# Optimization experiments

Measured on AMD Instinct MI355X. Metric: run time of the kernel, lower is better.

## Reference

```python
import jax, jax.numpy as jnp
import numpy as np


def setup_inputs() -> dict:
    key = jax.random.key(0)
    k1, k2, k3, k4 = jax.random.split(key, 4)
    B, T, E, H = 16, 2048, 1024, 128
    x = jax.random.normal(k1, (B, T, E), dtype=jnp.float32)
    Wk = jax.random.normal(k2, (E, H), dtype=jnp.float32) * (E ** -0.5)
    Wq = jax.random.normal(k3, (E, H), dtype=jnp.float32) * (E ** -0.5)
    Wv = jax.random.normal(k4, (E, H), dtype=jnp.float32) * (E ** -0.5)
    return {"x": x, "Wk": Wk, "Wq": Wq, "Wv": Wv}


def reference(x, Wk, Wq, Wv):
    # x: [B,T,E]; Wk/Wq/Wv: [E,H]
    B, T, E = x.shape
    H = Wk.shape[1]
    k = jnp.einsum('bte,eh->bth', x, Wk)
    q = jnp.einsum('bte,eh->bth', x, Wq)
    v = jnp.einsum('bte,eh->bth', x, Wv)
    # scores [B,T,T]; original masks with -inf THEN scales (equivalent math)
    scores = jnp.einsum('bqh,bkh->bqk', q, k) * (H ** -0.5)
    causal = jnp.tril(jnp.ones((T, T), dtype=bool))
    scores = jnp.where(causal, scores, -jnp.inf)
    weights = jax.nn.softmax(scores, axis=-1)
    # dropout disabled (eval mode reference)
    return jnp.einsum('bqk,bkh->bqh', weights, v)
```

## Files before the change

kernel.cpp:

```cpp
#include <hip/hip_runtime.h>

#define B_ 16
#define T_ 2048
#define E_ 1024
#define H_ 128

typedef short bf16x8 __attribute__((ext_vector_type(8)));
typedef float f32x4 __attribute__((ext_vector_type(4)));
typedef unsigned short u16x4 __attribute__((ext_vector_type(4)));

static __device__ __forceinline__ unsigned short f2bf(float f) {
    unsigned int u = __float_as_uint(f);
    u += 0x7FFFu + ((u >> 16) & 1u);
    return (unsigned short)(u >> 16);
}
static __device__ __forceinline__ unsigned int pk2(unsigned short a, unsigned short b) {
    return (unsigned int)a | ((unsigned int)b << 16);
}
static __device__ __forceinline__ bf16x8 frag(uint4 v) {
    return __builtin_bit_cast(bf16x8, v);
}
static __device__ __forceinline__ void gl16(const unsigned short* g, unsigned short* l) {
    __builtin_amdgcn_global_load_lds(
        (const __attribute__((address_space(1))) void*)g,
        (__attribute__((address_space(3))) void*)l, 16, 0, 0);
}

__global__ __launch_bounds__(256) void cvtw_kernel(
    const float* __restrict__ w0, const float* __restrict__ w1,
    const float* __restrict__ w2, unsigned short* __restrict__ wt)
{
    int g   = blockIdx.x * 256 + threadIdx.x;
    int arr = g >> 14;
    int rem = g & 16383;
    int h   = rem >> 7;
    int e0  = (rem & 127) * 8;
    const float* src = (arr == 0) ? w0 : (arr == 1) ? w1 : w2;
    unsigned short b[8];
#pragma unroll
    for (int i = 0; i < 8; i++) b[i] = f2bf(src[(size_t)(e0 + i) * H_ + h]);
    uint4 o;
    o.x = pk2(b[0], b[1]); o.y = pk2(b[2], b[3]);
    o.z = pk2(b[4], b[5]); o.w = pk2(b[6], b[7]);
    *(uint4*)&wt[(size_t)(arr * 128 + h) * E_ + e0] = o;
}

__global__ __launch_bounds__(512, 2) void proj_kernel(
    const float* __restrict__ x,
    const unsigned short* __restrict__ wt,
    unsigned short* __restrict__ q_ws,
    unsigned short* __restrict__ kp_ws,
    unsigned short* __restrict__ vt_ws)
{
    const int m0 = blockIdx.x * 128;
    __shared__ __align__(16) unsigned short As[2][128 * 32];
    __shared__ __align__(16) unsigned short Bs[2][384 * 32];

    const int tid  = threadIdx.x;
    const int lane = tid & 63;
    const int w    = tid >> 6;
    const int quad = lane >> 4;
    const int lm   = lane & 15;
    const int wr   = (w >> 2) * 64;
    const int wc   = (w & 3) * 96;

    const int srow = tid >> 2;
    const int scol = (tid & 3) * 8;
    const float* gx = x + (size_t)(m0 + srow) * E_ + scol;
    const unsigned short* gw = wt + (size_t)srow * E_ + scol;

    const f32x4 z4 = {0.f, 0.f, 0.f, 0.f};
    f32x4 acc[4][6];
#pragma unroll
    for (int i = 0; i < 4; i++)
#pragma unroll
        for (int j = 0; j < 6; j++) acc[i][j] = z4;

    auto stageB = [&](int kb, int buf) {
        const unsigned short* g = gw + kb * 32;
        unsigned short* l = &Bs[buf][tid * 8];
        gl16(g,                    l);
        gl16(g + (size_t)128 * E_, l + 4096);
        gl16(g + (size_t)256 * E_, l + 8192);
    };
    auto writeA = [&](float4 a0, float4 a1, int buf) {
        uint4 o;
        o.x = pk2(f2bf(a0.x), f2bf(a0.y));
        o.y = pk2(f2bf(a0.z), f2bf(a0.w));
        o.z = pk2(f2bf(a1.x), f2bf(a1.y));
        o.w = pk2(f2bf(a1.z), f2bf(a1.w));
        *(uint4*)&As[buf][srow * 32 + scol] = o;
    };

    float4 a0 = *(const float4*)gx;
    float4 a1 = *(const float4*)(gx + 4);
    stageB(0, 0);
    writeA(a0, a1, 0);
    a0 = *(const float4*)(gx + 32);
    a1 = *(const float4*)(gx + 36);

    for (int kb = 0; kb < 32; kb++) {
        const int cb = kb & 1;
        __syncthreads();

        const int kb2 = (kb + 2 < 32) ? kb + 2 : 31;
        float4 n0 = *(const float4*)(gx + kb2 * 32);
        float4 n1 = *(const float4*)(gx + kb2 * 32 + 4);
        if (kb + 1 < 32) {
            stageB(kb + 1, cb ^ 1);
            writeA(a0, a1, cb ^ 1);
        }

        bf16x8 a[4], b[6];
#pragma unroll
        for (int am = 0; am < 4; am++)
            a[am] = frag(*(const uint4*)&As[cb][(wr + am * 16 + lm) * 32 + quad * 8]);
#pragma unroll
        for (int bn = 0; bn < 6; bn++)
            b[bn] = frag(*(const uint4*)&Bs[cb][(wc + bn * 16 + lm) * 32 + quad * 8]);
#pragma unroll
        for (int am = 0; am < 4; am++)
#pragma unroll
            for (int bn = 0; bn < 6; bn++)
                acc[am][bn] = __builtin_amdgcn_mfma_f32_16x16x32_bf16(
                    a[am], b[bn], acc[am][bn], 0, 0, 0);

        a0 = n0; a1 = n1;
    }

#pragma unroll
    for (int am = 0; am < 4; am++)
#pragma unroll
        for (int bn = 0; bn < 6; bn++) {
            const int gcol  = wc + bn * 16 + lm;
            const int sel   = gcol >> 7;
            const int c     = gcol & 127;
            const int rbase = m0 + wr + am * 16 + quad * 4;
            const int bb    = rbase >> 11;
            const int t     = rbase & 2047;
            if (sel == 0) {
#pragma unroll
                for (int r = 0; r < 4; r++)
                    q_ws[(size_t)(rbase + r) * H_ + c] = f2bf(acc[am][bn][r]);
            } else if (sel == 1) {
#pragma unroll
                for (int r = 0; r < 4; r++) {
                    int tt = t + r;
                    kp_ws[(size_t)(bb * 64 + (tt >> 5)) * 4096 +
                          (c >> 5) * 1024 + (tt & 31) * 32 + (c & 31)] =
                        f2bf(acc[am][bn][r]);
                }
            } else {
                u16x4 pv;
#pragma unroll
                for (int r = 0; r < 4; r++) pv[r] = f2bf(acc[am][bn][r]);
                *(u16x4*)&vt_ws[((size_t)(bb * 64 + (t >> 5)) * 128 + c) * 32 + (t & 31)] = pv;
            }
        }
}

__global__ __launch_bounds__(256, 2) void attn_kernel(
    const unsigned short* __restrict__ q_ws,
    const unsigned short* __restrict__ kp_ws,
    const unsigned short* __restrict__ vt_ws,
    float* __restrict__ out)
{
    __shared__ __align__(16) unsigned short Ks[2][4096];
    __shared__ __align__(16) unsigned short Vs[2][4096];
    __shared__ __align__(16) unsigned short Ps[4][16][40];

    const int bid   = blockIdx.x;
    const int batch = bid & 15;
    const int p     = (bid >> 4) & 15;
    const int tau   = (bid >> 8) ? (31 - p) : p;
    const int nkt   = 2 * tau + 2;

    const int tid  = threadIdx.x;
    const int lane = tid & 63;
    const int ww   = tid >> 6;
    const int quad = lane >> 4;
    const int lm   = lane & 15;
    const float scale = 0.08838834764831845f;

    bf16x8 ones;
#pragma unroll
    for (int i = 0; i < 8; i++) ones[i] = (short)0x3F80;
    const f32x4 z4 = {0.f, 0.f, 0.f, 0.f};

    const size_t bq = (size_t)batch * T_ * H_;
    const int so = ww * 1024 + lane * 8;
    const unsigned short* Kt = kp_ws + (size_t)(batch * 64) * 4096 + so;
    const unsigned short* Vt = vt_ws + (size_t)(batch * 64) * 4096 + so;

    bf16x8 qf[4];
#pragma unroll
    for (int h = 0; h < 4; h++)
        qf[h] = frag(*(const uint4*)(q_ws + bq +
                 (size_t)(tau * 64 + ww * 16 + lm) * H_ + h * 32 + quad * 8));

    f32x4 o[9];
#pragma unroll
    for (int f = 0; f < 9; f++) o[f] = z4;

    gl16(Kt, &Ks[0][ww * 1024]); gl16(Kt + 512, &Ks[0][ww * 1024 + 512]);
    gl16(Vt, &Vs[0][ww * 1024]); gl16(Vt + 512, &Vs[0][ww * 1024 + 512]);

    for (int kt = 0; kt < nkt; kt++) {
        const int cb = kt & 1;
        __syncthreads();

        if (kt + 1 < nkt) {
            const int nb = cb ^ 1;
            const unsigned short* kg = Kt + (size_t)(kt + 1) * 4096;
            const unsigned short* vg = Vt + (size_t)(kt + 1) * 4096;
            gl16(kg, &Ks[nb][ww * 1024]); gl16(kg + 512, &Ks[nb][ww * 1024 + 512]);
            gl16(vg, &Vs[nb][ww * 1024]); gl16(vg + 512, &Vs[nb][ww * 1024 + 512]);
        }

        f32x4 st0 = z4, st1 = z4;
#pragma unroll
        for (int h = 0; h < 4; h++) {
            bf16x8 kf0 = frag(*(const uint4*)&Ks[cb][(h * 32 + lm) * 32 + quad * 8]);
            bf16x8 kf1 = frag(*(const uint4*)&Ks[cb][(h * 32 + 16 + lm) * 32 + quad * 8]);
            st0 = __builtin_amdgcn_mfma_f32_16x16x32_bf16(kf0, qf[h], st0, 0, 0, 0);
            st1 = __builtin_amdgcn_mfma_f32_16x16x32_bf16(kf1, qf[h], st1, 0, 0, 0);
        }

        const int qg = tau * 64 + ww * 16 + lm;
        const int k0 = kt * 32;
        u16x4 pa, pb;
#pragma unroll
        for (int r = 0; r < 4; r++) {
            int kv0 = k0 + quad * 4 + r;
            float e0 = __expf(st0[r] * scale);
            float e1 = __expf(st1[r] * scale);
            pa[r] = (kv0      <= qg) ? f2bf(e0) : (unsigned short)0;
            pb[r] = (kv0 + 16 <= qg) ? f2bf(e1) : (unsigned short)0;
        }
        *(u16x4*)&Ps[ww][lm][quad * 4]      = pa;
        *(u16x4*)&Ps[ww][lm][16 + quad * 4] = pb;
        bf16x8 pf = frag(*(const uint4*)&Ps[ww][lm][quad * 8]);

#pragma unroll
        for (int f = 0; f < 8; f++) {
            bf16x8 vfr = frag(*(const uint4*)&Vs[cb][(f * 16 + lm) * 32 + quad * 8]);
            o[f] = __builtin_amdgcn_mfma_f32_16x16x32_bf16(pf, vfr, o[f], 0, 0, 0);
        }
        o[8] = __builtin_amdgcn_mfma_f32_16x16x32_bf16(pf, ones, o[8], 0, 0, 0);
    }

    float* op = out + bq + (size_t)(tau * 64 + ww * 16) * H_;
#pragma unroll
    for (int r = 0; r < 4; r++) {
        float inv = 1.f / o[8][r];
#pragma unroll
        for (int f = 0; f < 8; f++)
            op[(size_t)(quad * 4 + r) * H_ + f * 16 + lm] = o[f][r] * inv;
    }
}

extern "C" void kernel_launch(void* const* d_in, const int* in_sizes, int n_in,
                              void* d_out, int out_size, void* d_ws, size_t ws_size,
                              hipStream_t stream)
{
    const float* x  = (const float*)d_in[0];
    const float* Wk = (const float*)d_in[1];
    const float* Wq = (const float*)d_in[2];
    const float* Wv = (const float*)d_in[3];
    float* out = (float*)d_out;

    const size_t MH = (size_t)B_ * T_ * H_;
    unsigned short* q_ws  = (unsigned short*)d_ws;
    unsigned short* kp_ws = q_ws + MH;
    unsigned short* vt_ws = kp_ws + MH;
    unsigned short* wt    = vt_ws + MH;

    cvtw_kernel<<<dim3(192), dim3(256), 0, stream>>>(Wq, Wk, Wv, wt);
    proj_kernel<<<dim3(256), dim3(512), 0, stream>>>(x, wt, q_ws, kp_ws, vt_ws);
    attn_kernel<<<dim3(512), dim3(256), 0, stream>>>(q_ws, kp_ws, vt_ws, out);
}
```

Baseline: 281.2 us.

## Shrink projection M-tile, load weight fragments directly from global, add MFMA priority hints

The projection kernel now uses 64-row tiles with 512 blocks. Each wave handles 48 output columns, and weight fragments are read straight from global memory (L2) into registers instead of being staged through shared memory. This removes the large B shared buffer and raises occupancy (launch bounds 4), at the cost of more redundant global weight reads per block and less reuse. The attention kernel also wraps its MFMA sections in s_setprio to favour matrix issue across waves.

```diff
diff --git a/kernel.cpp b/kernel.cpp
--- a/kernel.cpp
+++ b/kernel.cpp
@@ -45,97 +45,81 @@
     *(uint4*)&wt[(size_t)(arr * 128 + h) * E_ + e0] = o;
 }
 
-__global__ __launch_bounds__(512, 2) void proj_kernel(
+__global__ __launch_bounds__(512, 4) void proj_kernel(
     const float* __restrict__ x,
     const unsigned short* __restrict__ wt,
     unsigned short* __restrict__ q_ws,
     unsigned short* __restrict__ kp_ws,
     unsigned short* __restrict__ vt_ws)
 {
-    const int m0 = blockIdx.x * 128;
-    __shared__ __align__(16) unsigned short As[2][128 * 32];
-    __shared__ __align__(16) unsigned short Bs[2][384 * 32];
+    const int m0 = blockIdx.x * 64;
+    __shared__ __align__(16) unsigned short As[2][64 * 32];
 
     const int tid  = threadIdx.x;
     const int lane = tid & 63;
     const int w    = tid >> 6;
     const int quad = lane >> 4;
     const int lm   = lane & 15;
-    const int wr   = (w >> 2) * 64;
-    const int wc   = (w & 3) * 96;
-
-    const int srow = tid >> 2;
-    const int scol = (tid & 3) * 8;
+    const int wc   = w * 48;
+
+    const int srow = tid >> 3;
+    const int scol = (tid & 7) * 4;
     const float* gx = x + (size_t)(m0 + srow) * E_ + scol;
-    const unsigned short* gw = wt + (size_t)srow * E_ + scol;
+    const unsigned short* gb = wt + (size_t)(wc + lm) * E_ + quad * 8;
 
     const f32x4 z4 = {0.f, 0.f, 0.f, 0.f};
-    f32x4 acc[4][6];
+    f32x4 acc[4][3];
 #pragma unroll
     for (int i = 0; i < 4; i++)
 #pragma unroll
-        for (int j = 0; j < 6; j++) acc[i][j] = z4;
-
-    auto stageB = [&](int kb, int buf) {
-        const unsigned short* g = gw + kb * 32;
-        unsigned short* l = &Bs[buf][tid * 8];
-        gl16(g,                    l);
-        gl16(g + (size_t)128 * E_, l + 4096);
-        gl16(g + (size_t)256 * E_, l + 8192);
+        for (int j = 0; j < 3; j++) acc[i][j] = z4;
+
+    auto writeA = [&](float4 v, int buf) {
+        u16x4 o;
+        o[0] = f2bf(v.x); o[1] = f2bf(v.y);
+        o[2] = f2bf(v.z); o[3] = f2bf(v.w);
+        *(u16x4*)&As[buf][srow * 32 + scol] = o;
     };
-    auto writeA = [&](float4 a0, float4 a1, int buf) {
-        uint4 o;
-        o.x = pk2(f2bf(a0.x), f2bf(a0.y));
-        o.y = pk2(f2bf(a0.z), f2bf(a0.w));
-        o.z = pk2(f2bf(a1.x), f2bf(a1.y));
-        o.w = pk2(f2bf(a1.z), f2bf(a1.w));
-        *(uint4*)&As[buf][srow * 32 + scol] = o;
-    };
-
-    float4 a0 = *(const float4*)gx;
-    float4 a1 = *(const float4*)(gx + 4);
-    stageB(0, 0);
-    writeA(a0, a1, 0);
-    a0 = *(const float4*)(gx + 32);
-    a1 = *(const float4*)(gx + 36);
+
+    float4 a = *(const float4*)gx;
+    writeA(a, 0);
+    a = *(const float4*)(gx + 32);
 
     for (int kb = 0; kb < 32; kb++) {
         const int cb = kb & 1;
         __syncthreads();
 
+        uint4 b0 = *(const uint4*)(gb + (size_t)kb * 32);
+        uint4 b1 = *(const uint4*)(gb + (size_t)16 * E_ + (size_t)kb * 32);
+        uint4 b2 = *(const uint4*)(gb + (size_t)32 * E_ + (size_t)kb * 32);
+
         const int kb2 = (kb + 2 < 32) ? kb + 2 : 31;
-        float4 n0 = *(const float4*)(gx + kb2 * 32);
-        float4 n1 = *(const float4*)(gx + kb2 * 32 + 4);
-        if (kb + 1 < 32) {
-            stageB(kb + 1, cb ^ 1);
-            writeA(a0, a1, cb ^ 1);
-        }
-
-        bf16x8 a[4], b[6];
+        float4 n = *(const float4*)(gx + kb2 * 32);
+        if (kb + 1 < 32) writeA(a, cb ^ 1);
+
+        bf16x8 af[4];
 #pragma unroll
         for (int am = 0; am < 4; am++)
-            a[am] = frag(*(const uint4*)&As[cb][(wr + am * 16 + lm) * 32 + quad * 8]);
-#pragma unroll
-        for (int bn = 0; bn < 6; bn++)
-            b[bn] = frag(*(const uint4*)&Bs[cb][(wc + bn * 16 + lm) * 32 + quad * 8]);
-#pragma unroll
-        for (int am = 0; am < 4; am++)
-#pragma unroll
-            for (int bn = 0; bn < 6; bn++)
-                acc[am][bn] = __builtin_amdgcn_mfma_f32_16x16x32_bf16(
-                    a[am], b[bn], acc[am][bn], 0, 0, 0);
-
-        a0 = n0; a1 = n1;
+            af[am] = frag(*(const uint4*)&As[cb][(am * 16 + lm) * 32 + quad * 8]);
+
+        const bf16x8 bf0 = frag(b0), bf1 = frag(b1), bf2 = frag(b2);
+#pragma unroll
+        for (int am = 0; am < 4; am++) {
+            acc[am][0] = __builtin_amdgcn_mfma_f32_16x16x32_bf16(af[am], bf0, acc[am][0], 0, 0, 0);
+            acc[am][1] = __builtin_amdgcn_mfma_f32_16x16x32_bf16(af[am], bf1, acc[am][1], 0, 0, 0);
+            acc[am][2] = __builtin_amdgcn_mfma_f32_16x16x32_bf16(af[am], bf2, acc[am][2], 0, 0, 0);
+        }
+        a = n;
     }
 
 #pragma unroll
     for (int am = 0; am < 4; am++)
 #pragma unroll
-        for (int bn = 0; bn < 6; bn++) {
+        for (int bn = 0; bn < 3; bn++) {
             const int gcol  = wc + bn * 16 + lm;
             const int sel   = gcol >> 7;
             const int c     = gcol & 127;
-            const int rbase = m0 + wr + am * 16 + quad * 4;
+            const int rbase = m0 + am * 16 + quad * 4;
             const int bb    = rbase >> 11;
             const int t     = rbase & 2047;
             if (sel == 0) {
@@ -218,6 +202,7 @@
         }
 
         f32x4 st0 = z4, st1 = z4;
+        __builtin_amdgcn_s_setprio(1);
 #pragma unroll
         for (int h = 0; h < 4; h++) {
             bf16x8 kf0 = frag(*(const uint4*)&Ks[cb][(h * 32 + lm) * 32 + quad * 8]);
@@ -225,6 +210,7 @@
             st0 = __builtin_amdgcn_mfma_f32_16x16x32_bf16(kf0, qf[h], st0, 0, 0, 0);
             st1 = __builtin_amdgcn_mfma_f32_16x16x32_bf16(kf1, qf[h], st1, 0, 0, 0);
         }
+        __builtin_amdgcn_s_setprio(0);
 
         const int qg = tau * 64 + ww * 16 + lm;
         const int k0 = kt * 32;
@@ -241,12 +227,14 @@
         *(u16x4*)&Ps[ww][lm][16 + quad * 4] = pb;
         bf16x8 pf = frag(*(const uint4*)&Ps[ww][lm][quad * 8]);
 
+        __builtin_amdgcn_s_setprio(1);
 #pragma unroll
         for (int f = 0; f < 8; f++) {
             bf16x8 vfr = frag(*(const uint4*)&Vs[cb][(f * 16 + lm) * 32 + quad * 8]);
             o[f] = __builtin_amdgcn_mfma_f32_16x16x32_bf16(pf, vfr, o[f], 0, 0, 0);
         }
         o[8] = __builtin_amdgcn_mfma_f32_16x16x32_bf16(pf, ones, o[8], 0, 0, 0);
+        __builtin_amdgcn_s_setprio(0);
     }
 
     float* op = out + bq + (size_t)(tau * 64 + ww * 16) * H_;
@@ -276,6 +264,6 @@
     unsigned short* wt    = vt_ws + MH;
 
     cvtw_kernel<<<dim3(192), dim3(256), 0, stream>>>(Wq, Wk, Wv, wt);
-    proj_kernel<<<dim3(256), dim3(512), 0, stream>>>(x, wt, q_ws, kp_ws, vt_ws);
+    proj_kernel<<<dim3(512), dim3(512), 0, stream>>>(x, wt, q_ws, kp_ws, vt_ws);
     attn_kernel<<<dim3(512), dim3(256), 0, stream>>>(q_ws, kp_ws, vt_ws, out);
 }
```

Measured after the change: 288.3 us. 1.03x slower.

## Deepen prefetch pipelines in projection and attention kernels with explicit waitcnt barriers

Applied to the files above, without the earlier changes.

In the projection GEMM, the weight tile no longer goes through direct global-to-LDS loads. It is now loaded into registers along with the activation tile and prefetched three k-blocks ahead, with manual lgkmcnt waits and raw s_barrier instead of __syncthreads. The attention kernel moves from a double-buffered to a triple-buffered K/V pipeline. It waits on a partial vmcnt so two tiles can stay in flight, and raises wave priority around the MFMA sections. The goal is to hide global memory latency better, at the cost of more LDS, more registers, and fragile hand-written waitcnt logic.

```diff
diff --git a/kernel.cpp b/kernel.cpp
--- a/kernel.cpp
+++ b/kernel.cpp
@@ -76,56 +76,71 @@
 #pragma unroll
         for (int j = 0; j < 6; j++) acc[i][j] = z4;
 
-    auto stageB = [&](int kb, int buf) {
+    struct StA { float4 a0, a1; };
+    struct StB { uint4 b0, b1, b2; };
+
+    auto ldA = [&](int kb) {
+        StA r;
+        const float* g = gx + kb * 32;
+        r.a0 = *(const float4*)g;
+        r.a1 = *(const float4*)(g + 4);
+        return r;
+    };
+    auto ldB = [&](int kb) {
+        StB r;
         const unsigned short* g = gw + kb * 32;
-        unsigned short* l = &Bs[buf][tid * 8];
-        gl16(g,                    l);
-        gl16(g + (size_t)128 * E_, l + 4096);
-        gl16(g + (size_t)256 * E_, l + 8192);
+        r.b0 = *(const uint4*)g;
+        r.b1 = *(const uint4*)(g + (size_t)128 * E_);
+        r.b2 = *(const uint4*)(g + (size_t)256 * E_);
+        return r;
     };
-    auto writeA = [&](float4 a0, float4 a1, int buf) {
+    auto stAB = [&](const StA& a, const StB& b, int buf) {
         uint4 o;
-        o.x = pk2(f2bf(a0.x), f2bf(a0.y));
-        o.y = pk2(f2bf(a0.z), f2bf(a0.w));
-        o.z = pk2(f2bf(a1.x), f2bf(a1.y));
-        o.w = pk2(f2bf(a1.z), f2bf(a1.w));
-        *(uint4*)&As[buf][srow * 32 + scol] = o;
+        o.x = pk2(f2bf(a.a0.x), f2bf(a.a0.y));
+        o.y = pk2(f2bf(a.a0.z), f2bf(a.a0.w));
+        o.z = pk2(f2bf(a.a1.x), f2bf(a.a1.y));
+        o.w = pk2(f2bf(a.a1.z), f2bf(a.a1.w));
+        *(uint4*)&As[buf][srow * 32 + scol]        = o;
+        *(uint4*)&Bs[buf][srow * 32 + scol]        = b.b0;
+        *(uint4*)&Bs[buf][srow * 32 + scol + 4096] = b.b1;
+        *(uint4*)&Bs[buf][srow * 32 + scol + 8192] = b.b2;
     };
 
-    float4 a0 = *(const float4*)gx;
-    float4 a1 = *(const float4*)(gx + 4);
-    stageB(0, 0);
-    writeA(a0, a1, 0);
-    a0 = *(const float4*)(gx + 32);
-    a1 = *(const float4*)(gx + 36);
+    {
+        StA a0v = ldA(0); StB b0v = ldB(0);
+        stAB(a0v, b0v, 0);
+    }
+    StA a1v = ldA(1); StB b1v = ldB(1);
+    StA a2v = ldA(2); StB b2v = ldB(2);
 
     for (int kb = 0; kb < 32; kb++) {
         const int cb = kb & 1;
-        __syncthreads();
-
-        const int kb2 = (kb + 2 < 32) ? kb + 2 : 31;
-        float4 n0 = *(const float4*)(gx + kb2 * 32);
-        float4 n1 = *(const float4*)(gx + kb2 * 32 + 4);
-        if (kb + 1 < 32) {
-            stageB(kb + 1, cb ^ 1);
-            writeA(a0, a1, cb ^ 1);
-        }
+        asm volatile("s_waitcnt lgkmcnt(0)" ::: "memory");
+        __builtin_amdgcn_sched_barrier(0);
+        __builtin_amdgcn_s_barrier();
+        __builtin_amdgcn_sched_barrier(0);
+
+        const int kn = (kb + 3 < 32) ? kb + 3 : 31;
+        StA an = ldA(kn); StB bn = ldB(kn);
+
+        if (kb + 1 < 32) stAB(a1v, b1v, cb ^ 1);
 
         bf16x8 a[4], b[6];
 #pragma unroll
         for (int am = 0; am < 4; am++)
             a[am] = frag(*(const uint4*)&As[cb][(wr + am * 16 + lm) * 32 + quad * 8]);
 #pragma unroll
-        for (int bn = 0; bn < 6; bn++)
-            b[bn] = frag(*(const uint4*)&Bs[cb][(wc + bn * 16 + lm) * 32 + quad * 8]);
+        for (int bnn = 0; bnn < 6; bnn++)
+            b[bnn] = frag(*(const uint4*)&Bs[cb][(wc + bnn * 16 + lm) * 32 + quad * 8]);
 #pragma unroll
         for (int am = 0; am < 4; am++)
 #pragma unroll
-            for (int bn = 0; bn < 6; bn++)
-                acc[am][bn] = __builtin_amdgcn_mfma_f32_16x16x32_bf16(
-                    a[am], b[bn], acc[am][bn], 0, 0, 0);
-
-        a0 = n0; a1 = n1;
+            for (int bnn = 0; bnn < 6; bnn++)
+                acc[am][bnn] = __builtin_amdgcn_mfma_f32_16x16x32_bf16(
+                    a[am], b[bnn], acc[am][bnn], 0, 0, 0);
+
+        a1v = a2v; b1v = b2v;
+        a2v = an;  b2v = bn;
     }
 
 #pragma unroll
@@ -165,8 +180,8 @@
     const unsigned short* __restrict__ vt_ws,
     float* __restrict__ out)
 {
-    __shared__ __align__(16) unsigned short Ks[2][4096];
-    __shared__ __align__(16) unsigned short Vs[2][4096];
+    __shared__ __align__(16) unsigned short Ks[3][4096];
+    __shared__ __align__(16) unsigned short Vs[3][4096];
     __shared__ __align__(16) unsigned short Ps[4][16][40];
 
     const int bid   = blockIdx.x;
@@ -192,6 +207,15 @@
     const unsigned short* Kt = kp_ws + (size_t)(batch * 64) * 4096 + so;
     const unsigned short* Vt = vt_ws + (size_t)(batch * 64) * 4096 + so;
 
+    auto stage = [&](int t, int b) {
+        const unsigned short* kg = Kt + (size_t)t * 4096;
+        const unsigned short* vg = Vt + (size_t)t * 4096;
+        gl16(kg,       &Ks[b][ww * 1024]);
+        gl16(kg + 512, &Ks[b][ww * 1024 + 512]);
+        gl16(vg,       &Vs[b][ww * 1024]);
+        gl16(vg + 512, &Vs[b][ww * 1024 + 512]);
+    };
+
     bf16x8 qf[4];
 #pragma unroll
     for (int h = 0; h < 4; h++)
@@ -202,22 +226,21 @@
 #pragma unroll
     for (int f = 0; f < 9; f++) o[f] = z4;
 
-    gl16(Kt, &Ks[0][ww * 1024]); gl16(Kt + 512, &Ks[0][ww * 1024 + 512]);
-    gl16(Vt, &Vs[0][ww * 1024]); gl16(Vt + 512, &Vs[0][ww * 1024 + 512]);
+    stage(0, 0);
+    stage(1, 1);
 
     for (int kt = 0; kt < nkt; kt++) {
-        const int cb = kt & 1;
-        __syncthreads();
-
-        if (kt + 1 < nkt) {
-            const int nb = cb ^ 1;
-            const unsigned short* kg = Kt + (size_t)(kt + 1) * 4096;
-            const unsigned short* vg = Vt + (size_t)(kt + 1) * 4096;
-            gl16(kg, &Ks[nb][ww * 1024]); gl16(kg + 512, &Ks[nb][ww * 1024 + 512]);
-            gl16(vg, &Vs[nb][ww * 1024]); gl16(vg + 512, &Vs[nb][ww * 1024 + 512]);
-        }
+        const int cb = kt % 3;
+        asm volatile("s_waitcnt vmcnt(4) lgkmcnt(0)" ::: "memory");
+        __builtin_amdgcn_sched_barrier(0);
+        __builtin_amdgcn_s_barrier();
+        __builtin_amdgcn_sched_barrier(0);
+
+        int ks = kt + 2; if (ks > nkt - 1) ks = nkt - 1;
+        stage(ks, (kt + 2) % 3);
 
         f32x4 st0 = z4, st1 = z4;
+        __builtin_amdgcn_s_setprio(1);
 #pragma unroll
         for (int h = 0; h < 4; h++) {
             bf16x8 kf0 = frag(*(const uint4*)&Ks[cb][(h * 32 + lm) * 32 + quad * 8]);
@@ -225,6 +248,7 @@
             st0 = __builtin_amdgcn_mfma_f32_16x16x32_bf16(kf0, qf[h], st0, 0, 0, 0);
             st1 = __builtin_amdgcn_mfma_f32_16x16x32_bf16(kf1, qf[h], st1, 0, 0, 0);
         }
+        __builtin_amdgcn_s_setprio(0);
 
         const int qg = tau * 64 + ww * 16 + lm;
         const int k0 = kt * 32;
@@ -241,12 +265,14 @@
         *(u16x4*)&Ps[ww][lm][16 + quad * 4] = pb;
         bf16x8 pf = frag(*(const uint4*)&Ps[ww][lm][quad * 8]);
 
+        __builtin_amdgcn_s_setprio(1);
 #pragma unroll
         for (int f = 0; f < 8; f++) {
             bf16x8 vfr = frag(*(const uint4*)&Vs[cb][(f * 16 + lm) * 32 + quad * 8]);
             o[f] = __builtin_amdgcn_mfma_f32_16x16x32_bf16(pf, vfr, o[f], 0, 0, 0);
         }
         o[8] = __builtin_amdgcn_mfma_f32_16x16x32_bf16(pf, ones, o[8], 0, 0, 0);
+        __builtin_amdgcn_s_setprio(0);
     }
 
     float* op = out + bq + (size_t)(tau * 64 + ww * 16) * H_;
```

Measured after the change: 292.0 us. +3.9%, slower.

## Triple-buffer K/V tiles with counted vmcnt waits and MFMA priority boosts

Applied to the files above, without the earlier changes.

Moves the attention inner loop from double to triple buffering of K/V tiles in LDS. It prefetches two tiles ahead and waits with an explicit vmcnt(4) so that only the current tile's loads must have landed before the barrier. It also raises wave priority around the MFMA sections. The goal is to hide global-to-LDS load latency better. In exchange LDS use grows (about 49KB per block), which may limit occupancy at two blocks per CU. The loop also issues redundant clamped loads of the last tile near the end.

```diff
diff --git a/kernel.cpp b/kernel.cpp
--- a/kernel.cpp
+++ b/kernel.cpp
@@ -165,8 +165,8 @@
     const unsigned short* __restrict__ vt_ws,
     float* __restrict__ out)
 {
-    __shared__ __align__(16) unsigned short Ks[2][4096];
-    __shared__ __align__(16) unsigned short Vs[2][4096];
+    __shared__ __align__(16) unsigned short Ks[3][4096];
+    __shared__ __align__(16) unsigned short Vs[3][4096];
     __shared__ __align__(16) unsigned short Ps[4][16][40];
 
     const int bid   = blockIdx.x;
@@ -192,6 +192,15 @@
     const unsigned short* Kt = kp_ws + (size_t)(batch * 64) * 4096 + so;
     const unsigned short* Vt = vt_ws + (size_t)(batch * 64) * 4096 + so;
 
+    auto stage = [&](int t, int b) {
+        const unsigned short* kg = Kt + (size_t)t * 4096;
+        const unsigned short* vg = Vt + (size_t)t * 4096;
+        gl16(kg,       &Ks[b][ww * 1024]);
+        gl16(kg + 512, &Ks[b][ww * 1024 + 512]);
+        gl16(vg,       &Vs[b][ww * 1024]);
+        gl16(vg + 512, &Vs[b][ww * 1024 + 512]);
+    };
+
     bf16x8 qf[4];
 #pragma unroll
     for (int h = 0; h < 4; h++)
@@ -202,22 +211,21 @@
 #pragma unroll
     for (int f = 0; f < 9; f++) o[f] = z4;
 
-    gl16(Kt, &Ks[0][ww * 1024]); gl16(Kt + 512, &Ks[0][ww * 1024 + 512]);
-    gl16(Vt, &Vs[0][ww * 1024]); gl16(Vt + 512, &Vs[0][ww * 1024 + 512]);
+    stage(0, 0);
+    stage(1, 1);
 
     for (int kt = 0; kt < nkt; kt++) {
-        const int cb = kt & 1;
-        __syncthreads();
-
-        if (kt + 1 < nkt) {
-            const int nb = cb ^ 1;
-            const unsigned short* kg = Kt + (size_t)(kt + 1) * 4096;
-            const unsigned short* vg = Vt + (size_t)(kt + 1) * 4096;
-            gl16(kg, &Ks[nb][ww * 1024]); gl16(kg + 512, &Ks[nb][ww * 1024 + 512]);
-            gl16(vg, &Vs[nb][ww * 1024]); gl16(vg + 512, &Vs[nb][ww * 1024 + 512]);
-        }
+        const int cb = kt % 3;
+        asm volatile("s_waitcnt vmcnt(4) lgkmcnt(0)" ::: "memory");
+        __builtin_amdgcn_sched_barrier(0);
+        __builtin_amdgcn_s_barrier();
+        __builtin_amdgcn_sched_barrier(0);
+
+        int ks = kt + 2; if (ks > nkt - 1) ks = nkt - 1;
+        stage(ks, (kt + 2) % 3);
 
         f32x4 st0 = z4, st1 = z4;
+        __builtin_amdgcn_s_setprio(1);
 #pragma unroll
         for (int h = 0; h < 4; h++) {
             bf16x8 kf0 = frag(*(const uint4*)&Ks[cb][(h * 32 + lm) * 32 + quad * 8]);
@@ -225,6 +233,7 @@
             st0 = __builtin_amdgcn_mfma_f32_16x16x32_bf16(kf0, qf[h], st0, 0, 0, 0);
             st1 = __builtin_amdgcn_mfma_f32_16x16x32_bf16(kf1, qf[h], st1, 0, 0, 0);
         }
+        __builtin_amdgcn_s_setprio(0);
 
         const int qg = tau * 64 + ww * 16 + lm;
         const int k0 = kt * 32;
@@ -241,12 +250,14 @@
         *(u16x4*)&Ps[ww][lm][16 + quad * 4] = pb;
         bf16x8 pf = frag(*(const uint4*)&Ps[ww][lm][quad * 8]);
 
+        __builtin_amdgcn_s_setprio(1);
 #pragma unroll
         for (int f = 0; f < 8; f++) {
             bf16x8 vfr = frag(*(const uint4*)&Vs[cb][(f * 16 + lm) * 32 + quad * 8]);
             o[f] = __builtin_amdgcn_mfma_f32_16x16x32_bf16(pf, vfr, o[f], 0, 0, 0);
         }
         o[8] = __builtin_amdgcn_mfma_f32_16x16x32_bf16(pf, ones, o[8], 0, 0, 0);
+        __builtin_amdgcn_s_setprio(0);
     }
 
     float* op = out + bq + (size_t)(tau * 64 + ww * 16) * H_;
```

Result: no change. 281.7 us (+0.2%).
